# Kernel tuning notes

Measured on AMD Instinct MI355X. Metric: run time of the kernel, lower is better.

## Reference

```python
import jax, jax.numpy as jnp
import numpy as np
import math

EMB_DIM = 3        # positional embedding dim of the implicit Hyena filter
FILTER_ORDER = 64  # hidden width of the implicit filter MLP


def rmsnorm(x, w, eps=1e-8):
    return x * jax.lax.rsqrt(jnp.mean(x * x, axis=-1, keepdims=True) + eps) * w


def _implicit_filter(L, D, mlp_w1, mlp_b1, freq1, mlp_w2, mlp_b2, freq2, mlp_w3):
    # positional embedding (emb_dim=3): [t, Re exp(-i f w), Im exp(-i f w)], bands=1
    t = jnp.linspace(0.0, 1.0, L)[:, None]                               # (L,1)
    w = 2.0 * math.pi * jnp.linspace(0.0, L - 1.0, L)[:, None] / L       # (L,1)
    f = jnp.linspace(1e-4, 0.0, 1)[None, :]                              # (1,1)
    ang = f * w
    z = jnp.concatenate([t, jnp.cos(ang), -jnp.sin(ang)], axis=-1)       # (L,3)
    # implicit filter MLP with Sin activations
    h = jnp.sin(freq1 * (z @ mlp_w1.T + mlp_b1))
    h = jnp.sin(freq2 * (h @ mlp_w2.T + mlp_b2))
    h = h @ mlp_w3.T                                                     # (L,D)
    # exponential modulation (modulate=True)
    fast, slow, target = 0.3, 1.5, 1e-2
    max_decay = math.log(target) / fast
    min_decay = math.log(target) / slow
    deltas = jnp.linspace(min_decay, max_decay, D)[None, :]              # (1,D)
    h = h * jnp.exp(-t * jnp.abs(deltas))
    return h.T                                                           # (D,L)


def _fftconv(v, k, bias):
    # causal long conv via zero-padded FFT. v: (B,D,L), k: (D,L), bias: (D,)
    L = v.shape[-1]
    n = 2 * L
    kf = jnp.fft.rfft(k, n=n) / n
    y = jnp.fft.irfft(jnp.fft.rfft(v, n=n) * kf, n=n, norm="forward")[..., :L]
    return y + v * bias[None, :, None]


def _block(x, norm_in_w, in_proj_w, in_proj_b, short_filter_w, short_filter_b,
           mlp_w1, mlp_b1, freq1, mlp_w2, mlp_b2, freq2, mlp_w3, filter_bias,
           out_proj_w, out_proj_b, norm_w, ffn_w1, ffn_b1, ffn_w2, ffn_b2):
    B, L, D = x.shape
    xn = rmsnorm(x, norm_in_w)
    # Hyena operator
    u = (xn @ in_proj_w.T + in_proj_b).transpose(0, 2, 1)                # (B,3D,L)
    uc = jax.lax.conv_general_dilated(
        u, short_filter_w, (1,), [(2, 0)],
        feature_group_count=3 * D, dimension_numbers=("NCH", "OIH", "NCH"))
    uc = uc + short_filter_b[None, :, None]                              # causal k=3 depthwise
    x0, x1, v = jnp.split(uc, 3, axis=1)                                 # (B,D,L) each
    k = _implicit_filter(L, D, mlp_w1, mlp_b1, freq1, mlp_w2, mlp_b2, freq2, mlp_w3)
    v = _fftconv(v * x1, k, filter_bias)                                 # gate, long conv
    y = (v * x0).transpose(0, 2, 1) @ out_proj_w.T + out_proj_b          # gate, out proj
    # residual + FFN
    h = y + x
    o = rmsnorm(h, norm_w)
    o = jax.nn.gelu(o @ ffn_w1.T + ffn_b1) @ ffn_w2.T + ffn_b2
    return o + h


def setup_inputs():
    key = jax.random.key(0)
    B, L, D = 4, 2048, 1024
    ks = jax.random.split(key, 12)

    def lin(k, out_d, in_d):
        return jax.random.normal(k, (out_d, in_d), jnp.float32) * (1.0 / math.sqrt(in_d))

    return {
        "x": jax.random.normal(ks[0], (B, L, D), jnp.float32),
        "norm_in_w": jnp.ones((D,), jnp.float32),
        "in_proj_w": lin(ks[1], 3 * D, D),
        "in_proj_b": jnp.zeros((3 * D,), jnp.float32),
        "short_filter_w": jax.random.normal(ks[2], (3 * D, 1, 3), jnp.float32) / math.sqrt(3.0),
        "short_filter_b": jnp.zeros((3 * D,), jnp.float32),
        "mlp_w1": lin(ks[3], FILTER_ORDER, EMB_DIM),
        "mlp_b1": jnp.zeros((FILTER_ORDER,), jnp.float32),
        "freq1": jnp.ones((FILTER_ORDER,), jnp.float32),
        "mlp_w2": lin(ks[4], FILTER_ORDER, FILTER_ORDER),
        "mlp_b2": jnp.zeros((FILTER_ORDER,), jnp.float32),
        "freq2": jnp.ones((FILTER_ORDER,), jnp.float32),
        "mlp_w3": lin(ks[5], D, FILTER_ORDER),
        "filter_bias": jax.random.normal(ks[6], (D,), jnp.float32),
        "out_proj_w": lin(ks[7], D, D),
        "out_proj_b": jnp.zeros((D,), jnp.float32),
        "norm_w": jnp.ones((D,), jnp.float32),
        "ffn_w1": lin(ks[8], 2 * D, D),
        "ffn_b1": jnp.zeros((2 * D,), jnp.float32),
        "ffn_w2": lin(ks[9], D, 2 * D),
        "ffn_b2": jnp.zeros((D,), jnp.float32),
    }


def reference(x, norm_in_w, in_proj_w, in_proj_b, short_filter_w, short_filter_b,
              mlp_w1, mlp_b1, freq1, mlp_w2, mlp_b2, freq2, mlp_w3, filter_bias,
              out_proj_w, out_proj_b, norm_w, ffn_w1, ffn_b1, ffn_w2, ffn_b2):
    return _block(x, norm_in_w, in_proj_w, in_proj_b, short_filter_w, short_filter_b,
                  mlp_w1, mlp_b1, freq1, mlp_w2, mlp_b2, freq2, mlp_w3, filter_bias,
                  out_proj_w, out_proj_b, norm_w, ffn_w1, ffn_b1, ffn_w2, ffn_b2)
```

## Files before the change

### kernel.cpp

```cpp
#include <hip/hip_runtime.h>
#include <hip/hip_bf16.h>
#include <cstddef>

#define BB 4
#define LL 2048
#define DD 1024
#define MM (BB*LL)
#define KF_STRIDE 2056

#define SWZ(a) ((a) ^ (((a) >> 4) & 12))

typedef __bf16 bf16_t;
typedef __attribute__((ext_vector_type(8))) __bf16 bf16x8;
typedef __attribute__((ext_vector_type(4))) __bf16 bf16x4;
typedef __attribute__((ext_vector_type(4))) float f32x4;

#define GLD_LDS16(gp, lp) __builtin_amdgcn_global_load_lds(                 \
    (const __attribute__((address_space(1))) unsigned int*)(gp),            \
    (__attribute__((address_space(3))) unsigned int*)(lp), 16, 0, 0)

__device__ __forceinline__ float gelu_tanh(float x) {
    const float c = 0.7978845608028654f;
    float t = tanhf(c * (x + 0.044715f * x * x * x));
    return 0.5f * x * (1.0f + t);
}

__device__ __forceinline__ float2 cmul(float2 a, float2 b) {
    return make_float2(a.x * b.x - a.y * b.y, a.x * b.y + a.y * b.x);
}
__device__ __forceinline__ float2 cadd(float2 a, float2 b) {
    return make_float2(a.x + b.x, a.y + b.y);
}
__device__ __forceinline__ float2 csub(float2 a, float2 b) {
    return make_float2(a.x - b.x, a.y - b.y);
}
__device__ __forceinline__ float2 cmuli(float2 z, float s) {
    return make_float2(-s * z.y, s * z.x);
}

__global__ __launch_bounds__(256) void cast_all_kernel(
    const float* __restrict__ s0, const float* __restrict__ s1,
    const float* __restrict__ s2, const float* __restrict__ s3,
    bf16_t* __restrict__ d0, bf16_t* __restrict__ d1,
    bf16_t* __restrict__ d2, bf16_t* __restrict__ d3)
{
    const int b = blockIdx.x;
    const float* s; bf16_t* d; int base;
    if (b < 3072)      { s = s0; d = d0; base = b; }
    else if (b < 4096) { s = s1; d = d1; base = b - 3072; }
    else if (b < 6144) { s = s2; d = d2; base = b - 4096; }
    else               { s = s3; d = d3; base = b - 6144; }
    const int i = (base * 256 + threadIdx.x) * 4;
    const float4 v = *(const float4*)(s + i);
    bf16x4 o;
    o[0] = (bf16_t)v.x; o[1] = (bf16_t)v.y; o[2] = (bf16_t)v.z; o[3] = (bf16_t)v.w;
    *(bf16x4*)(d + i) = o;
}

__global__ __launch_bounds__(256) void rmsnorm_bf16_kernel(
    const float* __restrict__ in, const float* __restrict__ w,
    bf16_t* __restrict__ out)
{
    const int row = blockIdx.x;
    const float4* ip = (const float4*)(in + (size_t)row * DD);
    float4 v = ip[threadIdx.x];
    float ss = v.x*v.x + v.y*v.y + v.z*v.z + v.w*v.w;
    #pragma unroll
    for (int off = 32; off > 0; off >>= 1) ss += __shfl_down(ss, off, 64);
    __shared__ float sums[4];
    const int wid = threadIdx.x >> 6;
    if ((threadIdx.x & 63) == 0) sums[wid] = ss;
    __syncthreads();
    const float tot = sums[0] + sums[1] + sums[2] + sums[3];
    const float scale = rsqrtf(tot * (1.0f / (float)DD) + 1e-8f);
    const float4 wv = ((const float4*)w)[threadIdx.x];
    bf16x4 o;
    o[0] = (bf16_t)(v.x * scale * wv.x);
    o[1] = (bf16_t)(v.y * scale * wv.y);
    o[2] = (bf16_t)(v.z * scale * wv.z);
    o[3] = (bf16_t)(v.w * scale * wv.w);
    *(bf16x4*)(out + (size_t)row * DD + threadIdx.x * 4) = o;
}

template<int EPI, bool BF16OUT, bool BIASROW = false>
__global__ __launch_bounds__(256) void gemm_mfma_kernel(
    const bf16_t* __restrict__ A,
    const bf16_t* __restrict__ W,
    const float* __restrict__ bias,
    const float* __restrict__ res,
    float* __restrict__ Cf,
    bf16_t* __restrict__ Cb,
    int M, int N, int K)
{
    __shared__ __align__(16) bf16_t As[128 * 64];
    __shared__ __align__(16) bf16_t Ws[128 * 64];
    const int tid  = threadIdx.x;
    const int bm   = blockIdx.y * 128;
    const int bn   = blockIdx.x * 128;
    const int lane = tid & 63;
    const int wave = tid >> 6;
    const int wr   = (wave >> 1) * 64;
    const int wc   = (wave & 1) * 64;

    int srow[4], sqg[4];
    #pragma unroll
    for (int c = 0; c < 4; ++c) {
        const int p = c * 256 + tid;
        srow[c] = p >> 3;
        sqg[c]  = (((p & 7) ^ (srow[c] & 7)) << 3);
    }

    f32x4 acc[4][4] = {};

    const int fr = lane & 15;
    const int fc = (lane >> 4) * 8;

    for (int k0 = 0; k0 < K; k0 += 64) {
        #pragma unroll
        for (int c = 0; c < 4; ++c) {
            GLD_LDS16(A + (size_t)(bm + srow[c]) * K + k0 + sqg[c],
                      As + c * 2048 + tid * 8);
            GLD_LDS16(W + (size_t)(bn + srow[c]) * K + k0 + sqg[c],
                      Ws + c * 2048 + tid * 8);
        }
        __syncthreads();

        #pragma unroll
        for (int ks = 0; ks < 64; ks += 32) {
            const int q = (ks + fc) >> 3;
            bf16x8 af[4], wf[4];
            #pragma unroll
            for (int i = 0; i < 4; ++i) {
                const int r = wr + i*16 + fr;
                af[i] = *(const bf16x8*)(As + r * 64 + ((q ^ (r & 7)) << 3));
            }
            #pragma unroll
            for (int j = 0; j < 4; ++j) {
                const int r = wc + j*16 + fr;
                wf[j] = *(const bf16x8*)(Ws + r * 64 + ((q ^ (r & 7)) << 3));
            }
            #pragma unroll
            for (int i = 0; i < 4; ++i)
                #pragma unroll
                for (int j = 0; j < 4; ++j)
                    acc[i][j] = __builtin_amdgcn_mfma_f32_16x16x32_bf16(
                        af[i], wf[j], acc[i][j], 0, 0, 0);
        }
        __syncthreads();
    }

    const int fq = lane >> 4;
    #pragma unroll
    for (int i = 0; i < 4; ++i) {
        const int row0 = bm + wr + i*16 + fq*4;
        #pragma unroll
        for (int j = 0; j < 4; ++j) {
            const int col = bn + wc + j*16 + fr;
            const float bcol = BIASROW ? 0.0f : bias[col];
            #pragma unroll
            for (int r = 0; r < 4; ++r) {
                float v = acc[i][j][r] + (BIASROW ? bias[row0 + r] : bcol);
                if constexpr (EPI == 2) v = gelu_tanh(v);
                if constexpr (EPI == 1) v += res[(size_t)(row0 + r) * N + col];
                if constexpr (BF16OUT)
                    Cb[(size_t)(row0 + r) * N + col] = (bf16_t)v;
                else
                    Cf[(size_t)(row0 + r) * N + col] = v;
            }
        }
    }
}

__global__ __launch_bounds__(256) void shortfilter_kernel(
    const bf16_t* __restrict__ ut, const float* __restrict__ sw,
    const float* __restrict__ sb, bf16_t* __restrict__ x0t,
    float* __restrict__ vin)
{
    const int d = blockIdx.x;
    const int c0 = d, c1 = DD + d, c2 = 2 * DD + d;
    const float w0a = sw[c0*3+0], w0b = sw[c0*3+1], w0c = sw[c0*3+2], b0 = sb[c0];
    const float w1a = sw[c1*3+0], w1b = sw[c1*3+1], w1c = sw[c1*3+2], b1 = sb[c1];
    const float w2a = sw[c2*3+0], w2b = sw[c2*3+1], w2c = sw[c2*3+2], b2 = sb[c2];
    const bf16_t* r0 = ut + (size_t)c0 * MM;
    const bf16_t* r1 = ut + (size_t)c1 * MM;
    const bf16_t* r2 = ut + (size_t)c2 * MM;
    bf16_t* o0 = x0t + (size_t)d * MM;
    float*  o1 = vin + (size_t)d * MM;
    for (int m = threadIdx.x; m < MM; m += 256) {
        const int l = m & (LL - 1);
        float v0 = w0c * (float)r0[m] + b0;
        float v1 = w1c * (float)r1[m] + b1;
        float v2 = w2c * (float)r2[m] + b2;
        if (l >= 1) {
            v0 += w0b * (float)r0[m-1];
            v1 += w1b * (float)r1[m-1];
            v2 += w2b * (float)r2[m-1];
        }
        if (l >= 2) {
            v0 += w0a * (float)r0[m-2];
            v1 += w1a * (float)r1[m-2];
            v2 += w2a * (float)r2[m-2];
        }
        o0[m] = (bf16_t)v0;
        o1[m] = v2 * v1;
    }
}

__global__ __launch_bounds__(256) void filtermlp_kernel(
    const float* __restrict__ w1, const float* __restrict__ b1,
    const float* __restrict__ f1, const float* __restrict__ w2,
    const float* __restrict__ b2, const float* __restrict__ f2,
    float* __restrict__ h2t)
{
    __shared__ float w2s[64 * 64];
    __shared__ float h1s[64][32];
    const int tid = threadIdx.x;
    #pragma unroll
    for (int i = 0; i < 4; ++i)
        ((float4*)w2s)[tid + 256 * i] = ((const float4*)w2)[tid + 256 * i];

    const int l0 = blockIdx.x * 32;
    const int l  = tid & 31;
    const float fl = (float)(l0 + l);
    const float t   = fl * (1.0f / (float)(LL - 1));
    const float ang = 1e-4f * 6.283185307179586f * fl * (1.0f / (float)LL);
    const float z0 = t, z1 = cosf(ang), z2 = -sinf(ang);

    #pragma unroll
    for (int i = 0; i < 8; ++i) {
        const int j = (tid >> 5) + 8 * i;
        const float s = w1[j*3+0]*z0 + w1[j*3+1]*z1 + w1[j*3+2]*z2 + b1[j];
        h1s[j][l] = sinf(f1[j] * s);
    }
    __syncthreads();

    const int jb = (tid >> 5) * 8;
    float acc[8];
    #pragma unroll
    for (int i = 0; i < 8; ++i) acc[i] = b2[jb + i];
    #pragma unroll
    for (int jj = 0; jj < 64; jj += 4) {
        const float h0 = h1s[jj + 0][l];
        const float h1v = h1s[jj + 1][l];
        const float h2v = h1s[jj + 2][l];
        const float h3 = h1s[jj + 3][l];
        #pragma unroll
        for (int i = 0; i < 8; ++i) {
            const float4 wv = *(const float4*)&w2s[(jb + i) * 64 + jj];
            acc[i] += wv.x * h0 + wv.y * h1v + wv.z * h2v + wv.w * h3;
        }
    }
    #pragma unroll
    for (int i = 0; i < 8; ++i)
        h2t[(size_t)(jb + i) * LL + l0 + l] = sinf(f2[jb + i] * acc[i]);
}

__global__ __launch_bounds__(256) void filtermod_kernel(
    const float* __restrict__ w3, const float* __restrict__ h2t,
    float* __restrict__ kfilt)
{
    __shared__ float w3s[32 * 64];
    const int d0 = blockIdx.y * 32;
    const int l  = blockIdx.x * 256 + threadIdx.x;
    for (int i = threadIdx.x; i < 32 * 64; i += 256) w3s[i] = w3[d0 * 64 + i];
    __syncthreads();
    float acc[32] = {};
    for (int j = 0; j < 64; ++j) {
        const float v = h2t[j * LL + l];
        #pragma unroll
        for (int dd = 0; dd < 32; ++dd) acc[dd] += w3s[dd*64 + j] * v;
    }
    const float t = (float)l / (float)(LL - 1);
    const float min_decay = -3.0701134573253944f;
    const float max_decay = -15.350567286626972f;
    #pragma unroll
    for (int dd = 0; dd < 32; ++dd) {
        const int d = d0 + dd;
        const float delta = fabsf(min_decay + (max_decay - min_decay) * (float)d / (float)(DD - 1));
        kfilt[(size_t)d * LL + l] = acc[dd] * expf(-t * delta);
    }
}

template<int SIGN>
__device__ __forceinline__ void fft4096_r8_ip(float2* __restrict__ buf)
{
    const float fs = (float)SIGN;
    const float RH = 0.7071067811865476f;
    const int tid = threadIdx.x;
    #pragma unroll
    for (int t = 0; t < 4; ++t) {
        const int ls = 3 * t;
        const int s  = 1 << ls;
        const float theta = fs * 6.283185307179586f / (float)(4096 >> ls);
        float2 a[8];
        #pragma unroll
        for (int m = 0; m < 8; ++m) a[m] = buf[SWZ(tid + m * 512)];
        __syncthreads();
        const int p = tid >> ls;
        const int q = tid & (s - 1);
        float sn, cs;
        __sincosf(theta * (float)p, &sn, &cs);
        const float2 W1 = make_float2(cs, sn);
        const float2 W2 = cmul(W1, W1);
        const float2 W3 = cmul(W2, W1);
        const float2 W4 = cmul(W2, W2);
        const float2 W5 = cmul(W4, W1);
        const float2 W6 = cmul(W4, W2);
        const float2 W7 = cmul(W4, W3);
        const float2 es = cadd(a[0], a[4]), ed = csub(a[0], a[4]);
        const float2 fs2 = cadd(a[2], a[6]), fd = csub(a[2], a[6]);
        const float2 E0 = cadd(es, fs2);
        const float2 E1 = cadd(ed, cmuli(fd, fs));
        const float2 E2 = csub(es, fs2);
        const float2 E3 = csub(ed, cmuli(fd, fs));
        const float2 os = cadd(a[1], a[5]), od = csub(a[1], a[5]);
        const float2 gs = cadd(a[3], a[7]), gd = csub(a[3], a[7]);
        const float2 O0 = cadd(os, gs);
        const float2 O1 = cadd(od, cmuli(gd, fs));
        const float2 O2 = csub(os, gs);
        const float2 O3 = csub(od, cmuli(gd, fs));
        const float2 T0 = O0;
        const float2 T1 = make_float2(RH * (O1.x - fs * O1.y), RH * (fs * O1.x + O1.y));
        const float2 T2 = cmuli(O2, fs);
        const float2 T3 = make_float2(RH * (-O3.x - fs * O3.y), RH * (fs * O3.x - O3.y));
        const int o = q + (p << (ls + 3));
        buf[SWZ(o)]         = cadd(E0, T0);
        buf[SWZ(o + s)]     = cmul(W1, cadd(E1, T1));
        buf[SWZ(o + 2*s)]   = cmul(W2, cadd(E2, T2));
        buf[SWZ(o + 3*s)]   = cmul(W3, cadd(E3, T3));
        buf[SWZ(o + 4*s)]   = cmul(W4, csub(E0, T0));
        buf[SWZ(o + 5*s)]   = cmul(W5, csub(E1, T1));
        buf[SWZ(o + 6*s)]   = cmul(W6, csub(E2, T2));
        buf[SWZ(o + 7*s)]   = cmul(W7, csub(E3, T3));
        __syncthreads();
    }
}

__global__ __launch_bounds__(512, 4) void kfft_kernel(
    const float* __restrict__ kfilt, float2* __restrict__ Kf)
{
    __shared__ float2 fb[4096];
    const int d0 = blockIdx.x * 2;
    const float* k0 = kfilt + (size_t)d0 * LL;
    const float* k1 = k0 + LL;
    const float inv = 1.0f / 4096.0f;
    const int tid = threadIdx.x;
    for (int i = tid; i < 2048; i += 512) {
        fb[SWZ(i)]        = make_float2(k0[i] * inv, k1[i] * inv);
        fb[SWZ(i + 2048)] = make_float2(0.f, 0.f);
    }
    __syncthreads();
    fft4096_r8_ip<-1>(fb);
    float2* o0 = Kf + (size_t)d0 * KF_STRIDE;
    float2* o1 = o0 + KF_STRIDE;
    for (int k = tid; k <= 2048; k += 512) {
        const float2 z1 = fb[SWZ(k)];
        const float2 z2 = fb[SWZ((4096 - k) & 4095)];
        o0[k] = make_float2(0.5f * (z1.x + z2.x), 0.5f * (z1.y - z2.y));
        o1[k] = make_float2(0.5f * (z1.y + z2.y), 0.5f * (z2.x - z1.x));
    }
}

__global__ __launch_bounds__(512, 4) void fftconv_kernel(
    float* __restrict__ vio, const float2* __restrict__ Kf,
    const float* __restrict__ fbias)
{
    __shared__ float2 fb[4096];
    const int blk = blockIdx.x;
    const int d   = blk >> 1;
    float* v1 = vio + (size_t)(2 * blk) * LL;
    float* v2 = v1 + LL;
    const int tid = threadIdx.x;
    for (int i = tid; i < 2048; i += 512) {
        fb[SWZ(i)]        = make_float2(v1[i], v2[i]);
        fb[SWZ(i + 2048)] = make_float2(0.f, 0.f);
    }
    __syncthreads();
    fft4096_r8_ip<-1>(fb);
    const float2* kf = Kf + (size_t)d * KF_STRIDE;
    for (int i = tid; i < 4096; i += 512) {
        float2 k;
        if (i <= 2048) k = kf[i];
        else { const float2 t = kf[4096 - i]; k = make_float2(t.x, -t.y); }
        fb[SWZ(i)] = cmul(fb[SWZ(i)], k);
    }
    __syncthreads();
    fft4096_r8_ip<1>(fb);
    const float bias = fbias[d];
    for (int i = tid; i < 2048; i += 512) {
        const float2 zy = fb[SWZ(i)];
        v1[i] = zy.x + bias * v1[i];
        v2[i] = zy.y + bias * v2[i];
    }
}

__global__ __launch_bounds__(256) void gate_transpose_kernel(
    const float* __restrict__ y, const bf16_t* __restrict__ x0t,
    bf16_t* __restrict__ g)
{
    __shared__ float tile[32][33];
    const int b  = blockIdx.z;
    const int l0 = blockIdx.x * 32;
    const int d0 = blockIdx.y * 32;
    const int tx  = threadIdx.x & 31;
    const int tyb = threadIdx.x >> 5;
    #pragma unroll
    for (int i = 0; i < 4; ++i) {
        const int dy = tyb + i * 8;
        const size_t src = ((size_t)(d0 + dy) * BB + b) * LL + l0 + tx;
        tile[dy][tx] = y[src] * (float)x0t[src];
    }
    __syncthreads();
    #pragma unroll
    for (int i = 0; i < 4; ++i) {
        const int ly = tyb + i * 8;
        g[((size_t)(b * LL + l0 + ly)) * DD + d0 + tx] = (bf16_t)tile[tx][ly];
    }
}

extern "C" void kernel_launch(void* const* d_in, const int* in_sizes, int n_in,
                              void* d_out, int out_size, void* d_ws, size_t ws_size,
                              hipStream_t stream)
{
    (void)in_sizes; (void)n_in; (void)out_size; (void)ws_size;
    const float* x   = (const float*)d_in[0];
    const float* nw0 = (const float*)d_in[1];
    const float* ipw = (const float*)d_in[2];
    const float* ipb = (const float*)d_in[3];
    const float* sfw = (const float*)d_in[4];
    const float* sfb = (const float*)d_in[5];
    const float* w1  = (const float*)d_in[6];
    const float* b1  = (const float*)d_in[7];
    const float* f1  = (const float*)d_in[8];
    const float* w2  = (const float*)d_in[9];
    const float* b2  = (const float*)d_in[10];
    const float* f2  = (const float*)d_in[11];
    const float* w3  = (const float*)d_in[12];
    const float* fbv = (const float*)d_in[13];
    const float* opw = (const float*)d_in[14];
    const float* opb = (const float*)d_in[15];
    const float* nw1 = (const float*)d_in[16];
    const float* fw1 = (const float*)d_in[17];
    const float* fb1 = (const float*)d_in[18];
    const float* fw2 = (const float*)d_in[19];
    const float* fb2 = (const float*)d_in[20];
    float* out = (float*)d_out;

    float* ws = (float*)d_ws;
    bf16_t* utb    = (bf16_t*)ws;
    bf16_t* gatedb = (bf16_t*)ws;
    float*  h      = ws + 4194304;
    bf16_t* midb   = (bf16_t*)(ws + 12582912);
    bf16_t* xnb    = (bf16_t*)(ws + 25165824);
    bf16_t* x0tb   = (bf16_t*)(ws + 29360128);
    float*  vio    = ws + 37748736;
    float*  kfilt  = ws + 46137344;
    float2* Kf     = (float2*)(ws + 48234496);
    bf16_t* ipwb   = (bf16_t*)(ws + 52445184);
    bf16_t* opwb   = ipwb + 3145728;
    bf16_t* fw1b   = opwb + 1048576;
    bf16_t* fw2b   = fw1b + 2097152;
    float*  h2t    = ws + 56639488;

    cast_all_kernel<<<8192, 256, 0, stream>>>(ipw, opw, fw1, fw2,
                                              ipwb, opwb, fw1b, fw2b);
    filtermlp_kernel<<<LL/32, 256, 0, stream>>>(w1, b1, f1, w2, b2, f2, h2t);
    filtermod_kernel<<<dim3(LL/256, DD/32), 256, 0, stream>>>(w3, h2t, kfilt);
    kfft_kernel<<<DD/2, 512, 0, stream>>>(kfilt, Kf);
    rmsnorm_bf16_kernel<<<MM, 256, 0, stream>>>(x, nw0, xnb);
    gemm_mfma_kernel<0, true, true><<<dim3(MM/128, 3072/128), 256, 0, stream>>>(
        ipwb, xnb, ipb, nullptr, nullptr, utb, 3*DD, MM, DD);
    shortfilter_kernel<<<DD, 256, 0, stream>>>(utb, sfw, sfb, x0tb, vio);
    fftconv_kernel<<<BB*DD/2, 512, 0, stream>>>(vio, Kf, fbv);
    gate_transpose_kernel<<<dim3(LL/32, DD/32, BB), 256, 0, stream>>>(vio, x0tb, gatedb);
    gemm_mfma_kernel<1, false><<<dim3(DD/128, MM/128), 256, 0, stream>>>(
        gatedb, opwb, opb, x, h, nullptr, MM, DD, DD);
    rmsnorm_bf16_kernel<<<MM, 256, 0, stream>>>(h, nw1, xnb);
    gemm_mfma_kernel<2, true><<<dim3(2*DD/128, MM/128), 256, 0, stream>>>(
        xnb, fw1b, fb1, nullptr, nullptr, midb, MM, 2*DD, DD);
    gemm_mfma_kernel<1, false><<<dim3(DD/128, MM/128), 256, 0, stream>>>(
        midb, fw2b, fb2, h, out, nullptr, MM, DD, 2*DD);
}
```

Before: 503.4 us.

## Double-buffer GEMM LDS tiles and vectorize short-filter kernel

The MFMA GEMM now keeps two LDS buffers per operand and issues the global-to-LDS loads for the next K tile before computing on the current one, so memory latency overlaps compute with one barrier per tile. MFMA sections are raised in wave priority with s_setprio. Separately, the depthwise short-filter kernel now processes 8 elements per thread with 16-byte vector loads and stores instead of scalar bf16 accesses. LDS use per block doubles to 64 KB, which may lower occupancy. The one-barrier scheme may also be racy, since the next prefetch into a buffer is issued right after the barrier that follows its last reads, without a wait on the async loads.

```diff
diff --git a/kernel.cpp b/kernel.cpp
--- a/kernel.cpp
+++ b/kernel.cpp
@@ -92,8 +92,8 @@
     bf16_t* __restrict__ Cb,
     int M, int N, int K)
 {
-    __shared__ __align__(16) bf16_t As[128 * 64];
-    __shared__ __align__(16) bf16_t Ws[128 * 64];
+    __shared__ __align__(16) bf16_t As[2][128 * 64];
+    __shared__ __align__(16) bf16_t Ws[2][128 * 64];
     const int tid  = threadIdx.x;
     const int bm   = blockIdx.y * 128;
     const int bn   = blockIdx.x * 128;
@@ -115,16 +115,29 @@
     const int fr = lane & 15;
     const int fc = (lane >> 4) * 8;
 
-    for (int k0 = 0; k0 < K; k0 += 64) {
-        #pragma unroll
-        for (int c = 0; c < 4; ++c) {
-            GLD_LDS16(A + (size_t)(bm + srow[c]) * K + k0 + sqg[c],
-                      As + c * 2048 + tid * 8);
-            GLD_LDS16(W + (size_t)(bn + srow[c]) * K + k0 + sqg[c],
-                      Ws + c * 2048 + tid * 8);
-        }
-        __syncthreads();
-
+    const int nt = K >> 6;
+
+    #pragma unroll
+    for (int c = 0; c < 4; ++c) {
+        GLD_LDS16(A + (size_t)(bm + srow[c]) * K + sqg[c],
+                  &As[0][c * 2048 + tid * 8]);
+        GLD_LDS16(W + (size_t)(bn + srow[c]) * K + sqg[c],
+                  &Ws[0][c * 2048 + tid * 8]);
+    }
+    __syncthreads();
+
+    int cur = 0;
+    for (int t = 0; t < nt; ++t) {
+        if (t + 1 < nt) {
+            const int k0 = (t + 1) << 6;
+            #pragma unroll
+            for (int c = 0; c < 4; ++c) {
+                GLD_LDS16(A + (size_t)(bm + srow[c]) * K + k0 + sqg[c],
+                          &As[cur ^ 1][c * 2048 + tid * 8]);
+                GLD_LDS16(W + (size_t)(bn + srow[c]) * K + k0 + sqg[c],
+                          &Ws[cur ^ 1][c * 2048 + tid * 8]);
+            }
+        }
         #pragma unroll
         for (int ks = 0; ks < 64; ks += 32) {
             const int q = (ks + fc) >> 3;
@@ -132,21 +145,24 @@
             #pragma unroll
             for (int i = 0; i < 4; ++i) {
                 const int r = wr + i*16 + fr;
-                af[i] = *(const bf16x8*)(As + r * 64 + ((q ^ (r & 7)) << 3));
+                af[i] = *(const bf16x8*)(&As[cur][r * 64 + ((q ^ (r & 7)) << 3)]);
             }
             #pragma unroll
             for (int j = 0; j < 4; ++j) {
                 const int r = wc + j*16 + fr;
-                wf[j] = *(const bf16x8*)(Ws + r * 64 + ((q ^ (r & 7)) << 3));
+                wf[j] = *(const bf16x8*)(&Ws[cur][r * 64 + ((q ^ (r & 7)) << 3)]);
             }
+            __builtin_amdgcn_s_setprio(1);
             #pragma unroll
             for (int i = 0; i < 4; ++i)
                 #pragma unroll
                 for (int j = 0; j < 4; ++j)
                     acc[i][j] = __builtin_amdgcn_mfma_f32_16x16x32_bf16(
                         af[i], wf[j], acc[i][j], 0, 0, 0);
+            __builtin_amdgcn_s_setprio(0);
         }
         __syncthreads();
+        cur ^= 1;
     }
 
     const int fq = lane >> 4;
@@ -186,23 +202,37 @@
     const bf16_t* r2 = ut + (size_t)c2 * MM;
     bf16_t* o0 = x0t + (size_t)d * MM;
     float*  o1 = vin + (size_t)d * MM;
-    for (int m = threadIdx.x; m < MM; m += 256) {
-        const int l = m & (LL - 1);
-        float v0 = w0c * (float)r0[m] + b0;
-        float v1 = w1c * (float)r1[m] + b1;
-        float v2 = w2c * (float)r2[m] + b2;
-        if (l >= 1) {
-            v0 += w0b * (float)r0[m-1];
-            v1 += w1b * (float)r1[m-1];
-            v2 += w2b * (float)r2[m-1];
-        }
-        if (l >= 2) {
-            v0 += w0a * (float)r0[m-2];
-            v1 += w1a * (float)r1[m-2];
-            v2 += w2a * (float)r2[m-2];
-        }
-        o0[m] = (bf16_t)v0;
-        o1[m] = v2 * v1;
+    for (int m0 = threadIdx.x * 8; m0 < MM; m0 += 2048) {
+        const int l0 = m0 & (LL - 1);
+        const bf16x8 a0 = *(const bf16x8*)(r0 + m0);
+        const bf16x8 a1 = *(const bf16x8*)(r1 + m0);
+        const bf16x8 a2 = *(const bf16x8*)(r2 + m0);
+        float u0[10], u1[10], u2[10];
+        u0[0] = u0[1] = u1[0] = u1[1] = u2[0] = u2[1] = 0.0f;
+        if (l0 != 0) {
+            u0[0] = (float)r0[m0-2]; u0[1] = (float)r0[m0-1];
+            u1[0] = (float)r1[m0-2]; u1[1] = (float)r1[m0-1];
+            u2[0] = (float)r2[m0-2]; u2[1] = (float)r2[m0-1];
+        }
+        #pragma unroll
+        for (int i = 0; i < 8; ++i) {
+            u0[i+2] = (float)a0[i];
+            u1[i+2] = (float)a1[i];
+            u2[i+2] = (float)a2[i];
+        }
+        bf16x8 ov;
+        float v1o[8];
+        #pragma unroll
+        for (int i = 0; i < 8; ++i) {
+            const float v0 = w0c*u0[i+2] + w0b*u0[i+1] + w0a*u0[i] + b0;
+            const float v1 = w1c*u1[i+2] + w1b*u1[i+1] + w1a*u1[i] + b1;
+            const float v2 = w2c*u2[i+2] + w2b*u2[i+1] + w2a*u2[i] + b2;
+            ov[i] = (bf16_t)v0;
+            v1o[i] = v2 * v1;
+        }
+        *(bf16x8*)(o0 + m0) = ov;
+        *(float4*)(o1 + m0)     = make_float4(v1o[0], v1o[1], v1o[2], v1o[3]);
+        *(float4*)(o1 + m0 + 4) = make_float4(v1o[4], v1o[5], v1o[6], v1o[7]);
     }
 }
 
```

Result: faster. 481.5 us (-4.4%).
